# Optimization experiments

Hardware: AMD Instinct MI355X
Metric: run time of the kernel (lower is better)

## Reference

```python
import jax, jax.numpy as jnp
import numpy as np

B, D, H, N, M, K = 128, 256, 4, 256, 256, 10  # M=256 is hardcoded in the original repeat(1,1,1,256)
DIM = D // H  # per-head dim = 64


def setup_inputs() -> dict:
    key = jax.random.key(0)
    ks = jax.random.split(key, 10)
    s = 0.05  # weight scale
    return {
        "x": jax.random.normal(ks[0], (B, D, N), jnp.float32),
        "source": jax.random.normal(ks[1], (B, D, M), jnp.float32),
        "Wq": jax.random.normal(ks[2], (D, D), jnp.float32) * s,
        "bq": jax.random.normal(ks[3], (D,), jnp.float32) * s,
        "Wk": jax.random.normal(ks[4], (D, D), jnp.float32) * s,
        "bk": jax.random.normal(ks[5], (D,), jnp.float32) * s,
        "Wv": jax.random.normal(ks[6], (D, D), jnp.float32) * s,
        "bv": jax.random.normal(ks[7], (D,), jnp.float32) * s,
        "Wm": jax.random.normal(ks[8], (D, D), jnp.float32) * s,
        "bm": jax.random.normal(ks[9], (D,), jnp.float32) * s,
        "k": K,
    }


def _pointwise(W, b, x):
    # nn.Conv1d(d, d, kernel_size=1): per-point linear over channel dim
    return jnp.einsum('ef,bfn->ben', W, x) + b[None, :, None]


def reference(x, source, Wq, bq, Wk, bk, Wv, bv, Wm, bm, k):
    b, d, n = x.shape
    # torch .view(b, dim, heads, -1) splits channels as (dim, heads)
    q = _pointwise(Wq, bq, x).reshape(b, DIM, H, n)
    kk = _pointwise(Wk, bk, source).reshape(b, DIM, H, -1)
    v = _pointwise(Wv, bv, source).reshape(b, DIM, H, -1)

    scores = jnp.einsum('bdhn,bdhm->bhnm', q, kk) / jnp.sqrt(jnp.asarray(DIM, x.dtype))
    # per-row top-k threshold: keep only scores >= k-th largest, softmax over kept
    thresh = jax.lax.top_k(scores, k)[0][..., k - 1:k]  # [b,h,n,1]
    mask = scores >= thresh
    neg = jnp.finfo(scores.dtype).min
    prob = jax.nn.softmax(jnp.where(mask, scores, neg), axis=-1)
    prob = jnp.where(mask, prob, jnp.zeros((), scores.dtype))

    out = jnp.einsum('bhnm,bdhm->bdhn', prob, v).reshape(b, d, n)
    return _pointwise(Wm, bm, out)
```

## Files before the change

kernel.cpp:

```cpp
#include <hip/hip_runtime.h>
#include <hip/hip_bf16.h>

#define BB   128
#define DDIM 256
#define HH   4
#define NNN  256
#define MMM  256

typedef __hip_bfloat16 bf16;
typedef short  short8   __attribute__((ext_vector_type(8)));
typedef unsigned short ushort8_t __attribute__((ext_vector_type(8)));
typedef float  f32x4    __attribute__((ext_vector_type(4)));
typedef float  f32x2    __attribute__((ext_vector_type(2)));

__device__ __forceinline__ unsigned short f2bf(float x) {
    unsigned u = __builtin_bit_cast(unsigned, x);
    u += 0x7FFFu + ((u >> 16) & 1u);
    return (unsigned short)(u >> 16);
}
__device__ __forceinline__ float bf2f(unsigned short b) {
    unsigned u = ((unsigned)b) << 16;
    return __builtin_bit_cast(float, u);
}

__device__ __forceinline__ void xpose4(float v[4], const int p) {
    float ta = __shfl_xor((p & 1) ? v[0] : v[1], 1, 64);
    float tb = __shfl_xor((p & 1) ? v[2] : v[3], 1, 64);
    float u0 = (p & 1) ? ta : v[0];
    float u1 = (p & 1) ? v[1] : ta;
    float u2 = (p & 1) ? tb : v[2];
    float u3 = (p & 1) ? v[3] : tb;
    float tc = __shfl_xor((p & 2) ? u0 : u2, 2, 64);
    float td = __shfl_xor((p & 2) ? u1 : u3, 2, 64);
    v[0] = (p & 2) ? tc : u0;
    v[1] = (p & 2) ? td : u1;
    v[2] = (p & 2) ? u2 : tc;
    v[3] = (p & 2) ? u3 : td;
}

__device__ __forceinline__ void split3_store8k(char* dst, const float v[4]) {
    unsigned short h[4], m[4], l[4];
    #pragma unroll
    for (int i = 0; i < 4; ++i) {
        h[i] = f2bf(v[i]);
        float r1 = v[i] - bf2f(h[i]);
        m[i] = f2bf(r1);
        float r2 = r1 - bf2f(m[i]);
        l[i] = f2bf(r2);
    }
    uint2 hp, mp, lp;
    hp.x = (unsigned)h[0] | ((unsigned)h[1] << 16);
    hp.y = (unsigned)h[2] | ((unsigned)h[3] << 16);
    mp.x = (unsigned)m[0] | ((unsigned)m[1] << 16);
    mp.y = (unsigned)m[2] | ((unsigned)m[3] << 16);
    lp.x = (unsigned)l[0] | ((unsigned)l[1] << 16);
    lp.y = (unsigned)l[2] | ((unsigned)l[3] << 16);
    *(uint2*)dst = hp;
    *(uint2*)(dst + 8192) = mp;
    *(uint2*)(dst + 16384) = lp;
}

__device__ __forceinline__ void split2_store(char* dst, const float v[4]) {
    unsigned short h[4], m[4];
    #pragma unroll
    for (int i = 0; i < 4; ++i) {
        h[i] = f2bf(v[i]);
        float r1 = v[i] - bf2f(h[i]);
        m[i] = f2bf(r1);
    }
    uint2 hp, mp;
    hp.x = (unsigned)h[0] | ((unsigned)h[1] << 16);
    hp.y = (unsigned)h[2] | ((unsigned)h[3] << 16);
    mp.x = (unsigned)m[0] | ((unsigned)m[1] << 16);
    mp.y = (unsigned)m[2] | ((unsigned)m[3] << 16);
    *(uint2*)dst = hp;
    *(uint2*)(dst + 16384) = mp;
}

__device__ __forceinline__ void split1_store(char* dst, const float v[4]) {
    uint2 hp;
    hp.x = (unsigned)f2bf(v[0]) | ((unsigned)f2bf(v[1]) << 16);
    hp.y = (unsigned)f2bf(v[2]) | ((unsigned)f2bf(v[3]) << 16);
    *(uint2*)dst = hp;
}

__device__ __forceinline__ void ldx4(const float* p, float v[4]) {
    const float4 f = *(const float4*)p;
    v[0] = f.x; v[1] = f.y; v[2] = f.z; v[3] = f.w;
}
__device__ __forceinline__ void ldx4(const bf16* p, float v[4]) {
    uint2 u = *(const uint2*)p;
    v[0] = bf2f((unsigned short)(u.x & 0xFFFF));
    v[1] = bf2f((unsigned short)(u.x >> 16));
    v[2] = bf2f((unsigned short)(u.y & 0xFFFF));
    v[3] = bf2f((unsigned short)(u.y >> 16));
}

__device__ __forceinline__ float gmax16(float v) {
    v = fmaxf(v, __shfl_xor(v, 1, 64));
    v = fmaxf(v, __shfl_xor(v, 2, 64));
    v = fmaxf(v, __shfl_xor(v, 4, 64));
    v = fmaxf(v, __shfl_xor(v, 8, 64));
    return v;
}
__device__ __forceinline__ float gsum16(float v) {
    v += __shfl_xor(v, 1, 64);
    v += __shfl_xor(v, 2, 64);
    v += __shfl_xor(v, 4, 64);
    v += __shfl_xor(v, 8, 64);
    return v;
}

__device__ __forceinline__ void sort16_desc(float w[16]) {
    #pragma unroll
    for (int k = 2; k <= 16; k <<= 1) {
        #pragma unroll
        for (int j = k >> 1; j > 0; j >>= 1) {
            #pragma unroll
            for (int i = 0; i < 16; ++i) {
                const int l = i ^ j;
                if (l > i) {
                    const bool dmax = ((i & k) == 0);
                    float mx = fmaxf(w[i], w[l]);
                    float mn = fminf(w[i], w[l]);
                    w[i] = dmax ? mx : mn;
                    w[l] = dmax ? mn : mx;
                }
            }
        }
    }
}

__global__ __launch_bounds__(256)
void proj_kernel(const float* __restrict__ X, const float* __restrict__ W,
                 const float* __restrict__ bias, float* __restrict__ Y) {
    __shared__ float Wt[32][68];
    __shared__ float Xt[32][132];

    const int t  = threadIdx.x;
    const int tx = t & 31;
    const int ty = t >> 5;
    const int n0 = blockIdx.x * 128;
    const int e0 = blockIdx.y * 64;
    const int b  = blockIdx.z;
    const size_t plane = (size_t)b * DDIM * NNN;

    f32x2 acc2[8][2];
    #pragma unroll
    for (int i = 0; i < 8; ++i) {
        acc2[i][0] = f32x2{0.f, 0.f};
        acc2[i][1] = f32x2{0.f, 0.f};
    }

    for (int f0 = 0; f0 < DDIM; f0 += 32) {
        #pragma unroll
        for (int i = 0; i < 8; ++i) {
            int idx = t + i * 256;
            int fl = idx & 31, el = idx >> 5;
            Wt[fl][el] = W[(size_t)(e0 + el) * DDIM + f0 + fl];
        }
        #pragma unroll
        for (int i = 0; i < 4; ++i) {
            int idx = t + i * 256;
            int fl = idx >> 5, nl4 = idx & 31;
            *(float4*)&Xt[fl][nl4 * 4] =
                *(const float4*)&X[plane + (size_t)(f0 + fl) * NNN + n0 + nl4 * 4];
        }
        __syncthreads();

        #pragma unroll
        for (int ff = 0; ff < 32; ++ff) {
            const float4 av0 = *(const float4*)&Wt[ff][ty * 8];
            const float4 av1 = *(const float4*)&Wt[ff][ty * 8 + 4];
            const float4 bv  = *(const float4*)&Xt[ff][tx * 4];
            const float a[8] = {av0.x, av0.y, av0.z, av0.w, av1.x, av1.y, av1.z, av1.w};
            const f32x2 c0 = {bv.x, bv.y};
            const f32x2 c1 = {bv.z, bv.w};
            #pragma unroll
            for (int i2 = 0; i2 < 8; ++i2) {
                const f32x2 aa = {a[i2], a[i2]};
                acc2[i2][0] = __builtin_elementwise_fma(aa, c0, acc2[i2][0]);
                acc2[i2][1] = __builtin_elementwise_fma(aa, c1, acc2[i2][1]);
            }
        }
        __syncthreads();
    }

    #pragma unroll
    for (int i2 = 0; i2 < 8; ++i2) {
        const int e = e0 + ty * 8 + i2;
        const float bs = bias[e];
        const size_t off = plane + (size_t)e * NNN + n0 + tx * 4;
        float4 o;
        o.x = acc2[i2][0].x + bs; o.y = acc2[i2][0].y + bs;
        o.z = acc2[i2][1].x + bs; o.w = acc2[i2][1].y + bs;
        *(float4*)&Y[off] = o;
    }
}

__global__ __launch_bounds__(256)
void projk_kernel(const float* __restrict__ X, const float* __restrict__ W,
                  const float* __restrict__ bias,
                  unsigned short* __restrict__ Ph, unsigned short* __restrict__ Pm,
                  unsigned short* __restrict__ Pl) {
    __shared__ float Wt[32][268];
    __shared__ float Xt[32][36];

    const int t  = threadIdx.x;
    const int tx = t & 7;
    const int ty = t >> 3;
    const int n0 = blockIdx.x * 32;
    const int b  = blockIdx.y;
    const size_t plane = (size_t)b * DDIM * NNN;

    f32x2 acc2[8][2];
    #pragma unroll
    for (int i = 0; i < 8; ++i) {
        acc2[i][0] = f32x2{0.f, 0.f};
        acc2[i][1] = f32x2{0.f, 0.f};
    }

    for (int f0 = 0; f0 < DDIM; f0 += 32) {
        #pragma unroll
        for (int i = 0; i < 8; ++i) {
            int idx = t + i * 256;
            int fq = idx & 7, el = idx >> 3;
            const float4 w4 = *(const float4*)&W[(size_t)el * DDIM + f0 + fq * 4];
            Wt[fq * 4 + 0][el] = w4.x;
            Wt[fq * 4 + 1][el] = w4.y;
            Wt[fq * 4 + 2][el] = w4.z;
            Wt[fq * 4 + 3][el] = w4.w;
        }
        #pragma unroll
        for (int i = 0; i < 4; ++i) {
            int idx = t + i * 256;
            int fl = idx >> 5, nl = idx & 31;
            Xt[fl][nl] = X[plane + (size_t)(f0 + fl) * NNN + n0 + nl];
        }
        __syncthreads();

        #pragma unroll
        for (int ff = 0; ff < 32; ++ff) {
            const float4 av0 = *(const float4*)&Wt[ff][ty * 8];
            const float4 av1 = *(const float4*)&Wt[ff][ty * 8 + 4];
            const float4 bv  = *(const float4*)&Xt[ff][tx * 4];
            const float a[8] = {av0.x, av0.y, av0.z, av0.w, av1.x, av1.y, av1.z, av1.w};
            const f32x2 c0 = {bv.x, bv.y};
            const f32x2 c1 = {bv.z, bv.w};
            #pragma unroll
            for (int i2 = 0; i2 < 8; ++i2) {
                const f32x2 aa = {a[i2], a[i2]};
                acc2[i2][0] = __builtin_elementwise_fma(aa, c0, acc2[i2][0]);
                acc2[i2][1] = __builtin_elementwise_fma(aa, c1, acc2[i2][1]);
            }
        }
        __syncthreads();
    }

    float* stage = &Wt[0][0];
    #pragma unroll
    for (int i2 = 0; i2 < 8; ++i2) {
        const int e = ty * 8 + i2;
        const float bs = bias[e];
        const int col = (e & 3) * 64 + (e >> 2);
        stage[(tx * 4 + 0) * 260 + col] = acc2[i2][0].x + bs;
        stage[(tx * 4 + 1) * 260 + col] = acc2[i2][0].y + bs;
        stage[(tx * 4 + 2) * 260 + col] = acc2[i2][1].x + bs;
        stage[(tx * 4 + 3) * 260 + col] = acc2[i2][1].y + bs;
    }
    __syncthreads();

    #pragma unroll
    for (int it = 0; it < 8; ++it) {
        int gid = t + it * 256;
        int n   = gid >> 6;
        int sub = gid & 63;
        const float4 v4 = *(const float4*)&stage[n * 260 + sub * 4];
        const int hh = sub >> 4;
        const int dd0 = (sub & 15) * 4;
        const size_t off = ((size_t)(b * 4 + hh) * NNN + n0 + n) * 64 + dd0;
        const float v[4] = {v4.x, v4.y, v4.z, v4.w};
        unsigned short h[4], m[4], l[4];
        #pragma unroll
        for (int i = 0; i < 4; ++i) {
            h[i] = f2bf(v[i]);
            float r1 = v[i] - bf2f(h[i]);
            m[i] = f2bf(r1);
            float r2 = r1 - bf2f(m[i]);
            l[i] = f2bf(r2);
        }
        uint2 hp, mp, lp;
        hp.x = (unsigned)h[0] | ((unsigned)h[1] << 16);
        hp.y = (unsigned)h[2] | ((unsigned)h[3] << 16);
        mp.x = (unsigned)m[0] | ((unsigned)m[1] << 16);
        mp.y = (unsigned)m[2] | ((unsigned)m[3] << 16);
        lp.x = (unsigned)l[0] | ((unsigned)l[1] << 16);
        lp.y = (unsigned)l[2] | ((unsigned)l[3] << 16);
        *(uint2*)&Ph[off] = hp;
        *(uint2*)&Pm[off] = mp;
        *(uint2*)&Pl[off] = lp;
    }
}

__global__ __launch_bounds__(256, 4)
void attn4_kernel(const float* __restrict__ qf,
                  const unsigned short* __restrict__ khp,
                  const unsigned short* __restrict__ kmp,
                  const unsigned short* __restrict__ klp,
                  const bf16* __restrict__ vb, bf16* __restrict__ ob,
                  const int* __restrict__ kptr) {
    extern __shared__ __align__(16) char smem[];

    const int t    = threadIdx.x;
    const int lane = t & 63;
    const int w    = t >> 6;
    const int g    = lane >> 4;
    const int c16  = lane & 15;

    const int i    = blockIdx.x;
    const int work = (i & 7) * 256 + (i >> 3);
    const int bx = work & 3;
    const int h  = (work >> 2) & 3;
    const int b  = work >> 4;
    const int n0 = bx * 64;
    const int bh = b * 4 + h;

    const size_t planeF = (size_t)b * DDIM * NNN;
    const size_t planeV = (size_t)b * DDIM * MMM;

    int kk = kptr[0];
    kk = kk < 1 ? 1 : (kk > MMM ? MMM : kk);

    {
        const int p = lane & 3, G = lane >> 2;
        #pragma unroll
        for (int it = 0; it < 4; ++it) {
            int dch = w + 4 * it;
            int drow = dch * 4 + p;
            float v[4];
            const float4 f4 = *(const float4*)&qf[planeF + (size_t)(drow * HH + h) * NNN + n0 + G * 4];
            v[0] = f4.x * 0.125f; v[1] = f4.y * 0.125f;
            v[2] = f4.z * 0.125f; v[3] = f4.w * 0.125f;
            xpose4(v, p);
            int nl = G * 4 + p;
            int base = nl * 128 + ((dch * 8) ^ ((nl & 7) << 4));
            split3_store8k(smem + base, v);
        }
    }
    __syncthreads();

    short8 qh[2], qm[2], ql[2];
    #pragma unroll
    for (int ks = 0; ks < 2; ++ks) {
        int nl = w * 16 + c16;
        int off = nl * 128 + ((ks * 64 + g * 16) ^ ((nl & 7) << 4));
        qh[ks] = *(const short8*)(smem + off);
        qm[ks] = *(const short8*)(smem + 8192 + off);
        ql[ks] = *(const short8*)(smem + 16384 + off);
    }
    __syncthreads();

    f32x4 acc[16];
    #pragma unroll
    for (int m = 0; m < 16; ++m) acc[m] = f32x4{0.f, 0.f, 0.f, 0.f};

    #pragma unroll
    for (int tt = 0; tt < 4; ++tt) {
        if (tt) __syncthreads();
        #pragma unroll
        for (int it = 0; it < 6; ++it) {
            int gid = t + it * 256;
            int pl  = gid >> 9;
            int rem = gid & 511;
            int ml  = rem >> 3;
            int dq  = rem & 7;
            int dqs = dq ^ (ml & 7);
            const unsigned short* kp = (pl == 0) ? khp : (pl == 1 ? kmp : klp);
            const unsigned short* src = kp + ((size_t)bh * MMM + tt * 64 + ml) * 64 + dqs * 8;
            __builtin_amdgcn_global_load_lds(
                (const __attribute__((address_space(1))) void*)src,
                (__attribute__((address_space(3))) void*)(smem + gid * 16),
                16, 0, 0);
        }
        __syncthreads();

        #pragma unroll
        for (int mf = 0; mf < 4; ++mf) {
            #pragma unroll
            for (int ks = 0; ks < 2; ++ks) {
                int ml = mf * 16 + c16;
                int off = ml * 128 + ((ks * 64 + g * 16) ^ ((ml & 7) << 4));
                short8 bh_ = *(const short8*)(smem + off);
                short8 bm_ = *(const short8*)(smem + 8192 + off);
                short8 bl_ = *(const short8*)(smem + 16384 + off);
                f32x4 a = acc[tt * 4 + mf];
                a = __builtin_amdgcn_mfma_f32_16x16x32_bf16(qh[ks], bh_, a, 0, 0, 0);
                a = __builtin_amdgcn_mfma_f32_16x16x32_bf16(qh[ks], bm_, a, 0, 0, 0);
                a = __builtin_amdgcn_mfma_f32_16x16x32_bf16(qm[ks], bh_, a, 0, 0, 0);
                a = __builtin_amdgcn_mfma_f32_16x16x32_bf16(qm[ks], bm_, a, 0, 0, 0);
                a = __builtin_amdgcn_mfma_f32_16x16x32_bf16(qh[ks], bl_, a, 0, 0, 0);
                a = __builtin_amdgcn_mfma_f32_16x16x32_bf16(ql[ks], bh_, a, 0, 0, 0);
                acc[tt * 4 + mf] = a;
            }
        }
    }
    __syncthreads();

    float thr[4], rmx[4];
    #pragma unroll
    for (int r = 0; r < 4; ++r) {
        float s[16];
        #pragma unroll
        for (int mf = 0; mf < 16; ++mf) s[mf] = acc[mf][r];
        sort16_desc(s);
        float gm = gmax16(s[0]);
        rmx[r] = gm;
        for (int it = 1; it < kk; ++it) {
            unsigned long long bal = __ballot(s[0] == gm);
            unsigned gmask = (unsigned)((bal >> (g * 16)) & 0xFFFFull);
            int leader = __builtin_ctz(gmask);
            bool hit = (c16 == leader);
            #pragma unroll
            for (int j = 0; j < 15; ++j) s[j] = hit ? s[j + 1] : s[j];
            s[15] = hit ? -INFINITY : s[15];
            gm = gmax16(s[0]);
        }
        thr[r] = gm;
    }

    #pragma unroll
    for (int mf = 0; mf < 16; ++mf) {
        #pragma unroll
        for (int r = 0; r < 4; ++r) {
            float a = acc[mf][r];
            acc[mf][r] = (a >= thr[r]) ? __expf(a - rmx[r]) : 0.f;
        }
    }
    float inv_[4];
    #pragma unroll
    for (int r = 0; r < 4; ++r) {
        float s = ((acc[0][r] + acc[1][r]) + (acc[2][r] + acc[3][r]))
                + ((acc[4][r] + acc[5][r]) + (acc[6][r] + acc[7][r]))
                + ((acc[8][r] + acc[9][r]) + (acc[10][r] + acc[11][r]))
                + ((acc[12][r] + acc[13][r]) + (acc[14][r] + acc[15][r]));
        s = gsum16(s);
        inv_[r] = 1.0f / s;
    }
    #pragma unroll
    for (int mf = 0; mf < 16; ++mf) {
        #pragma unroll
        for (int r = 0; r < 4; ++r) {
            int row = w * 16 + g * 4 + r;
            int m2  = (mf * 16 + c16) * 2;
            int off = row * 512 + (m2 ^ ((row & 7) << 4));
            *(unsigned short*)(smem + off) = f2bf(acc[mf][r] * inv_[r]);
        }
    }
    __syncthreads();

    f32x4 o[4];
    #pragma unroll
    for (int df = 0; df < 4; ++df) o[df] = f32x4{0.f, 0.f, 0.f, 0.f};

    #pragma unroll
    for (int half = 0; half < 2; ++half) {
        short8 pa[4];
        #pragma unroll
        for (int ks = 0; ks < 4; ++ks) {
            int row = w * 16 + c16;
            int off = row * 512 + ((half * 256 + ks * 64 + g * 16) ^ ((row & 7) << 4));
            pa[ks] = *(const short8*)(smem + off);
        }
        #pragma unroll
        for (int df = 0; df < 4; ++df) {
            int d = df * 16 + c16;
            const bf16* vrow = vb + planeV + (size_t)(d * HH + h) * MMM + half * 128;
            f32x4 o_ = o[df];
            #pragma unroll
            for (int ks = 0; ks < 4; ++ks) {
                short8 vv = *(const short8*)(vrow + ks * 32 + g * 8);
                o_ = __builtin_amdgcn_mfma_f32_16x16x32_bf16(pa[ks], vv, o_, 0, 0, 0);
            }
            o[df] = o_;
        }
    }
    __syncthreads();

    #pragma unroll
    for (int df = 0; df < 4; ++df)
        #pragma unroll
        for (int r = 0; r < 4; ++r) {
            int d  = df * 16 + c16;
            int nl = w * 16 + g * 4 + r;
            int off = d * 128 + ((nl * 2) ^ ((d & 7) << 4));
            *(unsigned short*)(smem + off) = f2bf(o[df][r]);
        }
    __syncthreads();
    #pragma unroll
    for (int it = 0; it < 2; ++it) {
        int idx = t + it * 256;
        int d = idx >> 3, ch = idx & 7;
        int off = d * 128 + ((ch * 16) ^ ((d & 7) << 4));
        ushort8_t val = *(const ushort8_t*)(smem + off);
        *(ushort8_t*)&ob[planeV + (size_t)(d * HH + h) * NNN + n0 + ch * 8] = val;
    }
}

template <typename TIN, typename TOUT>
__global__ __launch_bounds__(512, 2)
void projm_kernel(const TIN* __restrict__ X, const float* __restrict__ W,
                  const float* __restrict__ bias, TOUT* __restrict__ Y) {
    extern __shared__ __align__(16) char smem[];
    constexpr bool XBF = (sizeof(TIN) == 2);
    constexpr int WOFF = XBF ? 16384 : 32768;

    const int t    = threadIdx.x;
    const int lane = t & 63;
    const int w    = t >> 6;
    const int c16  = lane & 15;
    const int g    = (lane >> 4) & 3;
    const int p    = lane & 3;
    const int G    = lane >> 2;

    const int n0 = blockIdx.x * 128;
    const int e0 = blockIdx.y * 128;
    const int b  = blockIdx.z;
    const size_t plane = (size_t)b * DDIM * NNN;

    f32x4 acc[8];
    #pragma unroll
    for (int nf = 0; nf < 8; ++nf) acc[nf] = f32x4{0.f, 0.f, 0.f, 0.f};

    #pragma unroll
    for (int ft = 0; ft < 4; ++ft) {
        const int f0 = ft * 64;
        if (ft) __syncthreads();
        #pragma unroll
        for (int it = 0; it < 4; ++it) {
            int chunk = w + 8 * it;
            int fch = chunk & 15, nh = chunk >> 4;
            float v[4];
            ldx4(&X[plane + (size_t)(f0 + fch * 4 + p) * NNN + n0 + nh * 64 + G * 4], v);
            xpose4(v, p);
            int nl = nh * 64 + G * 4 + p;
            int base = nl * 128 + ((fch * 8) ^ ((nl & 7) << 4));
            if constexpr (XBF) split1_store(smem + base, v);
            else               split2_store(smem + base, v);
        }
        #pragma unroll
        for (int it = 0; it < 4; ++it) {
            int idx = t + 512 * it;
            int el = idx >> 4, fq = idx & 15;
            float v[4];
            const float4 f4 = *(const float4*)&W[(size_t)(e0 + el) * DDIM + f0 + fq * 4];
            v[0] = f4.x; v[1] = f4.y; v[2] = f4.z; v[3] = f4.w;
            int base = WOFF + el * 128 + ((fq * 8) ^ ((el & 7) << 4));
            split2_store(smem + base, v);
        }
        __syncthreads();

        const int ew = w * 16;
        short8 a0[2], a1[2];
        #pragma unroll
        for (int ks = 0; ks < 2; ++ks) {
            int off = WOFF + (ew + c16) * 128
                    + ((ks * 64 + g * 16) ^ ((c16 & 7) << 4));
            a0[ks] = *(const short8*)(smem + off);
            a1[ks] = *(const short8*)(smem + off + 16384);
        }
        #pragma unroll
        for (int nf = 0; nf < 8; ++nf) {
            #pragma unroll
            for (int ks = 0; ks < 2; ++ks) {
                int off = (nf * 16 + c16) * 128
                        + ((ks * 64 + g * 16) ^ ((c16 & 7) << 4));
                short8 b0 = *(const short8*)(smem + off);
                f32x4 a = acc[nf];
                a = __builtin_amdgcn_mfma_f32_16x16x32_bf16(a0[ks], b0, a, 0, 0, 0);
                if constexpr (!XBF) {
                    short8 b1 = *(const short8*)(smem + off + 16384);
                    a = __builtin_amdgcn_mfma_f32_16x16x32_bf16(a0[ks], b1, a, 0, 0, 0);
                }
                a = __builtin_amdgcn_mfma_f32_16x16x32_bf16(a1[ks], b0, a, 0, 0, 0);
                acc[nf] = a;
            }
        }
    }

    const int ew = w * 16;
    float bs[4];
    #pragma unroll
    for (int r = 0; r < 4; ++r) bs[r] = bias[e0 + ew + g * 4 + r];
    #pragma unroll
    for (int nf = 0; nf < 8; ++nf) {
        #pragma unroll
        for (int r = 0; r < 4; ++r) {
            size_t off = plane + (size_t)(e0 + ew + g * 4 + r) * NNN + n0 + nf * 16 + c16;
            float val = acc[nf][r] + bs[r];
            if constexpr (sizeof(TOUT) == 4) Y[off] = val;
            else                             *(unsigned short*)&Y[off] = f2bf(val);
        }
    }
}

extern "C" void kernel_launch(void* const* d_in, const int* in_sizes, int n_in,
                              void* d_out, int out_size, void* d_ws, size_t ws_size,
                              hipStream_t stream) {
    const float* x   = (const float*)d_in[0];
    const float* src = (const float*)d_in[1];
    const float* Wq  = (const float*)d_in[2];
    const float* bq  = (const float*)d_in[3];
    const float* Wk  = (const float*)d_in[4];
    const float* bk  = (const float*)d_in[5];
    const float* Wv  = (const float*)d_in[6];
    const float* bv  = (const float*)d_in[7];
    const float* Wm  = (const float*)d_in[8];
    const float* bm  = (const float*)d_in[9];
    const int*   kp  = (const int*)d_in[10];
    float* out = (float*)d_out;

    char* ws = (char*)d_ws;
    const size_t QF_BYTES = 33554432;
    const size_t PL_BYTES = 16777216;

    float*          qf = (float*)(ws);
    unsigned short* kh = (unsigned short*)(ws + QF_BYTES);
    unsigned short* km = (unsigned short*)(ws + QF_BYTES + PL_BYTES);
    unsigned short* kl = (unsigned short*)(ws + QF_BYTES + 2 * PL_BYTES);
    bf16*           vb = (bf16*)(ws + QF_BYTES + 3 * PL_BYTES);
    bf16*           ob = (bf16*)(ws + QF_BYTES + 4 * PL_BYTES);

    hipFuncSetAttribute((const void*)(projm_kernel<float, bf16>),
                        hipFuncAttributeMaxDynamicSharedMemorySize, 65536);
    hipFuncSetAttribute((const void*)(projm_kernel<bf16, float>),
                        hipFuncAttributeMaxDynamicSharedMemorySize, 49152);
    hipFuncSetAttribute((const void*)attn4_kernel,
                        hipFuncAttributeMaxDynamicSharedMemorySize, 32768);

    dim3 qgrid(NNN / 128, DDIM / 64, BB);
    dim3 kgrid(NNN / 32, BB);
    dim3 mgrid(2, 2, BB);

    hipLaunchKernelGGL(proj_kernel, qgrid, dim3(256), 0, stream,
                       x,   Wq, bq, qf);
    hipLaunchKernelGGL(projk_kernel, kgrid, dim3(256), 0, stream,
                       src, Wk, bk, kh, km, kl);
    hipLaunchKernelGGL((projm_kernel<float, bf16>), mgrid, dim3(512), 65536, stream,
                       src, Wv, bv, vb);
    hipLaunchKernelGGL(attn4_kernel, dim3(2048), dim3(256), 32768, stream,
                       qf, kh, km, kl, vb, ob, kp);
    hipLaunchKernelGGL((projm_kernel<bf16, float>), mgrid, dim3(512), 49152, stream,
                       ob, Wm, bm, out);
}
```

Baseline: 251.4 us.

## Retile K projection to 128x64 output tiles with split epilogue staging

The K projection kernel now computes 128 output channels by 64 points per block instead of all 256 channels by 32 points, using a 3D grid over point tiles, channel halves and batch. X tiles are loaded as float4 and the weight tile as scalar transposed loads. The epilogue stages results through shared memory in two halves to fit the smaller buffer before splitting into three bf16 planes. This halves per-block shared memory and changes how often weights and inputs are reused, at the cost of reloading X for each channel half and an extra pair of barriers.

```diff
diff --git a/kernel.cpp b/kernel.cpp
--- a/kernel.cpp
+++ b/kernel.cpp
@@ -203,14 +203,15 @@
                   const float* __restrict__ bias,
                   unsigned short* __restrict__ Ph, unsigned short* __restrict__ Pm,
                   unsigned short* __restrict__ Pl) {
-    __shared__ float Wt[32][268];
-    __shared__ float Xt[32][36];
+    __shared__ float Wt[32][132];
+    __shared__ float Xt[32][68];
 
     const int t  = threadIdx.x;
-    const int tx = t & 7;
-    const int ty = t >> 3;
-    const int n0 = blockIdx.x * 32;
-    const int b  = blockIdx.y;
+    const int tx = t & 15;
+    const int ty = t >> 4;
+    const int n0 = blockIdx.x * 64;
+    const int e0 = blockIdx.y * 128;
+    const int b  = blockIdx.z;
     const size_t plane = (size_t)b * DDIM * NNN;
 
     f32x2 acc2[8][2];
@@ -222,20 +223,17 @@
 
     for (int f0 = 0; f0 < DDIM; f0 += 32) {
         #pragma unroll
-        for (int i = 0; i < 8; ++i) {
+        for (int i = 0; i < 16; ++i) {
             int idx = t + i * 256;
-            int fq = idx & 7, el = idx >> 3;
-            const float4 w4 = *(const float4*)&W[(size_t)el * DDIM + f0 + fq * 4];
-            Wt[fq * 4 + 0][el] = w4.x;
-            Wt[fq * 4 + 1][el] = w4.y;
-            Wt[fq * 4 + 2][el] = w4.z;
-            Wt[fq * 4 + 3][el] = w4.w;
-        }
-        #pragma unroll
-        for (int i = 0; i < 4; ++i) {
+            int fl = idx & 31, el = idx >> 5;
+            Wt[fl][el] = W[(size_t)(e0 + el) * DDIM + f0 + fl];
+        }
+        #pragma unroll
+        for (int i = 0; i < 2; ++i) {
             int idx = t + i * 256;
-            int fl = idx >> 5, nl = idx & 31;
-            Xt[fl][nl] = X[plane + (size_t)(f0 + fl) * NNN + n0 + nl];
+            int fl = idx >> 4, nl4 = idx & 15;
+            *(float4*)&Xt[fl][nl4 * 4] =
+                *(const float4*)&X[plane + (size_t)(f0 + fl) * NNN + n0 + nl4 * 4];
         }
         __syncthreads();
 
@@ -257,48 +255,60 @@
         __syncthreads();
     }
 
-    float* stage = &Wt[0][0];
-    #pragma unroll
-    for (int i2 = 0; i2 < 8; ++i2) {
-        const int e = ty * 8 + i2;
-        const float bs = bias[e];
-        const int col = (e & 3) * 64 + (e >> 2);
-        stage[(tx * 4 + 0) * 260 + col] = acc2[i2][0].x + bs;
-        stage[(tx * 4 + 1) * 260 + col] = acc2[i2][0].y + bs;
-        stage[(tx * 4 + 2) * 260 + col] = acc2[i2][1].x + bs;
-        stage[(tx * 4 + 3) * 260 + col] = acc2[i2][1].y + bs;
-    }
-    __syncthreads();
-
-    #pragma unroll
-    for (int it = 0; it < 8; ++it) {
-        int gid = t + it * 256;
-        int n   = gid >> 6;
-        int sub = gid & 63;
-        const float4 v4 = *(const float4*)&stage[n * 260 + sub * 4];
-        const int hh = sub >> 4;
-        const int dd0 = (sub & 15) * 4;
-        const size_t off = ((size_t)(b * 4 + hh) * NNN + n0 + n) * 64 + dd0;
-        const float v[4] = {v4.x, v4.y, v4.z, v4.w};
-        unsigned short h[4], m[4], l[4];
-        #pragma unroll
-        for (int i = 0; i < 4; ++i) {
-            h[i] = f2bf(v[i]);
-            float r1 = v[i] - bf2f(h[i]);
-            m[i] = f2bf(r1);
-            float r2 = r1 - bf2f(m[i]);
-            l[i] = f2bf(r2);
-        }
-        uint2 hp, mp, lp;
-        hp.x = (unsigned)h[0] | ((unsigned)h[1] << 16);
-        hp.y = (unsigned)h[2] | ((unsigned)h[3] << 16);
-        mp.x = (unsigned)m[0] | ((unsigned)m[1] << 16);
-        mp.y = (unsigned)m[2] | ((unsigned)m[3] << 16);
-        lp.x = (unsigned)l[0] | ((unsigned)l[1] << 16);
-        lp.y = (unsigned)l[2] | ((unsigned)l[3] << 16);
-        *(uint2*)&Ph[off] = hp;
-        *(uint2*)&Pm[off] = mp;
-        *(uint2*)&Pl[off] = lp;
+    float bsv[8];
+    #pragma unroll
+    for (int i2 = 0; i2 < 8; ++i2) bsv[i2] = bias[e0 + ty * 8 + i2];
+
+    float* sbuf = &Wt[0][0];
+    #pragma unroll
+    for (int hf = 0; hf < 2; ++hf) {
+        if ((tx >> 3) == hf) {
+            #pragma unroll
+            for (int i2 = 0; i2 < 8; ++i2) {
+                const int e = e0 + ty * 8 + i2;
+                const int col = (e & 3) * 32 + ((e >> 2) - (e0 >> 2));
+                const float vals[4] = {acc2[i2][0].x + bsv[i2], acc2[i2][0].y + bsv[i2],
+                                       acc2[i2][1].x + bsv[i2], acc2[i2][1].y + bsv[i2]};
+                const int nb = (tx - hf * 8) * 4;
+                sbuf[(nb + 0) * 132 + col] = vals[0];
+                sbuf[(nb + 1) * 132 + col] = vals[1];
+                sbuf[(nb + 2) * 132 + col] = vals[2];
+                sbuf[(nb + 3) * 132 + col] = vals[3];
+            }
+        }
+        __syncthreads();
+        #pragma unroll
+        for (int it = 0; it < 4; ++it) {
+            int u  = t + it * 256;
+            int c4 = u & 31;
+            int n  = u >> 5;
+            const float4 v4 = *(const float4*)&sbuf[n * 132 + c4 * 4];
+            const int hh = c4 >> 3;
+            const int dq = c4 & 7;
+            const size_t off = ((size_t)(b * 4 + hh) * NNN + n0 + hf * 32 + n) * 64
+                             + (e0 >> 2) + dq * 4;
+            const float v[4] = {v4.x, v4.y, v4.z, v4.w};
+            unsigned short h[4], m[4], l[4];
+            #pragma unroll
+            for (int i = 0; i < 4; ++i) {
+                h[i] = f2bf(v[i]);
+                float r1 = v[i] - bf2f(h[i]);
+                m[i] = f2bf(r1);
+                float r2 = r1 - bf2f(m[i]);
+                l[i] = f2bf(r2);
+            }
+            uint2 hp, mp, lp;
+            hp.x = (unsigned)h[0] | ((unsigned)h[1] << 16);
+            hp.y = (unsigned)h[2] | ((unsigned)h[3] << 16);
+            mp.x = (unsigned)m[0] | ((unsigned)m[1] << 16);
+            mp.y = (unsigned)m[2] | ((unsigned)m[3] << 16);
+            lp.x = (unsigned)l[0] | ((unsigned)l[1] << 16);
+            lp.y = (unsigned)l[2] | ((unsigned)l[3] << 16);
+            *(uint2*)&Ph[off] = hp;
+            *(uint2*)&Pm[off] = mp;
+            *(uint2*)&Pl[off] = lp;
+        }
+        __syncthreads();
     }
 }
 
@@ -638,7 +648,7 @@
                         hipFuncAttributeMaxDynamicSharedMemorySize, 32768);
 
     dim3 qgrid(NNN / 128, DDIM / 64, BB);
-    dim3 kgrid(NNN / 32, BB);
+    dim3 kgrid(NNN / 64, DDIM / 128, BB);
     dim3 mgrid(2, 2, BB);
 
     hipLaunchKernelGGL(proj_kernel, qgrid, dim3(256), 0, stream,
```

After: 247.9 us. No clear change (-1.4%).
